# Optimization experiments

Hardware: AMD Instinct MI355X
Metric: run time of the kernel (lower is better)

## Reference

```python
import jax, jax.numpy as jnp
import numpy as np

H = 8   # n_heads
C = 2   # top-k scale factor: topk = int(C * log(L))


def setup_inputs() -> dict:
    key = jax.random.key(0)
    k1, k2, k3 = jax.random.split(key, 3)
    B, L, D = 16, 512, 4096  # L == D // H required by the original broadcasting
    Q = jax.random.normal(k1, (B, L, D), dtype=jnp.float32)
    K = jax.random.normal(k2, (B, L, D), dtype=jnp.float32)
    V = jax.random.normal(k3, (B, L, D), dtype=jnp.float32)
    return {"Q": Q, "K": K, "V": V}


def _autocorrelation(Q, K, V):
    B, L, D = Q.shape
    d = D // H
    # [B,L,D] -> [B,H,L,d]
    q = Q.reshape(B, L, H, d).transpose(0, 2, 1, 3)
    k = K.reshape(B, L, H, d).transpose(0, 2, 1, 3)
    v = V.reshape(B, L, H, d).transpose(0, 2, 1, 3)
    # FFT-based autocorrelation along the time axis (per head, per channel)
    qf = jnp.fft.fft(q, axis=2)
    kf = jnp.fft.fft(k, axis=2)
    corr = jnp.fft.ifft(qf * jnp.conj(kf), axis=2).real  # [B,H,L,d]
    topk = int(C * np.log(L))  # static: 12 for L=512
    # top-k delays per (batch, head, channel): move L to last axis
    w, idx = jax.lax.top_k(corr.transpose(0, 1, 3, 2), topk)  # [B,H,d,topk]
    w = jax.nn.softmax(w, axis=-1)
    pos = jnp.arange(L)[:, None]  # [L,1]
    out = jnp.zeros_like(v)       # [B,H,L,d]
    # small fixed loop over topk ~ O(log L) delays: gather + scale + accumulate
    for i in range(topk):
        g = jnp.minimum(idx[:, :, None, :, i] + pos, L - 1)        # [B,H,L,d]
        out = out + w[:, :, None, :, i] * jnp.take_along_axis(v, g, axis=2)
    return out.transpose(0, 2, 1, 3).reshape(B, L, D)


def reference(Q, K, V):
    return _autocorrelation(Q, K, V)
```

## Files before the change

### kernel.cpp

```cpp
#include <hip/hip_runtime.h>
#include <stdint.h>

#define L_LEN 512
#define D_DIM 4096
#define H_NUM 8
#define B_NUM 16
#define TOPK  12

typedef float f32x4 __attribute__((ext_vector_type(4)));


#define QA(G) (qbase + (((((uint32_t)(G)) & 127u) + ((((uint32_t)(G)) & 127u) >> 3)) << 4))

#define MAC4x16(QA_, QB_, QC_, QD_, QE_, KK_) do {                            \
    acc0  = fmaf(QA_.x, KK_.x, acc0);  acc0  = fmaf(QA_.y, KK_.y, acc0);      \
    acc0  = fmaf(QA_.z, KK_.z, acc0);  acc0  = fmaf(QA_.w, KK_.w, acc0);      \
    acc1  = fmaf(QA_.y, KK_.x, acc1);  acc1  = fmaf(QA_.z, KK_.y, acc1);      \
    acc1  = fmaf(QA_.w, KK_.z, acc1);  acc1  = fmaf(QB_.x, KK_.w, acc1);      \
    acc2  = fmaf(QA_.z, KK_.x, acc2);  acc2  = fmaf(QA_.w, KK_.y, acc2);      \
    acc2  = fmaf(QB_.x, KK_.z, acc2);  acc2  = fmaf(QB_.y, KK_.w, acc2);      \
    acc3  = fmaf(QA_.w, KK_.x, acc3);  acc3  = fmaf(QB_.x, KK_.y, acc3);      \
    acc3  = fmaf(QB_.y, KK_.z, acc3);  acc3  = fmaf(QB_.z, KK_.w, acc3);      \
    acc4  = fmaf(QB_.x, KK_.x, acc4);  acc4  = fmaf(QB_.y, KK_.y, acc4);      \
    acc4  = fmaf(QB_.z, KK_.z, acc4);  acc4  = fmaf(QB_.w, KK_.w, acc4);      \
    acc5  = fmaf(QB_.y, KK_.x, acc5);  acc5  = fmaf(QB_.z, KK_.y, acc5);      \
    acc5  = fmaf(QB_.w, KK_.z, acc5);  acc5  = fmaf(QC_.x, KK_.w, acc5);      \
    acc6  = fmaf(QB_.z, KK_.x, acc6);  acc6  = fmaf(QB_.w, KK_.y, acc6);      \
    acc6  = fmaf(QC_.x, KK_.z, acc6);  acc6  = fmaf(QC_.y, KK_.w, acc6);      \
    acc7  = fmaf(QB_.w, KK_.x, acc7);  acc7  = fmaf(QC_.x, KK_.y, acc7);      \
    acc7  = fmaf(QC_.y, KK_.z, acc7);  acc7  = fmaf(QC_.z, KK_.w, acc7);      \
    acc8  = fmaf(QC_.x, KK_.x, acc8);  acc8  = fmaf(QC_.y, KK_.y, acc8);      \
    acc8  = fmaf(QC_.z, KK_.z, acc8);  acc8  = fmaf(QC_.w, KK_.w, acc8);      \
    acc9  = fmaf(QC_.y, KK_.x, acc9);  acc9  = fmaf(QC_.z, KK_.y, acc9);      \
    acc9  = fmaf(QC_.w, KK_.z, acc9);  acc9  = fmaf(QD_.x, KK_.w, acc9);      \
    acc10 = fmaf(QC_.z, KK_.x, acc10); acc10 = fmaf(QC_.w, KK_.y, acc10);     \
    acc10 = fmaf(QD_.x, KK_.z, acc10); acc10 = fmaf(QD_.y, KK_.w, acc10);     \
    acc11 = fmaf(QC_.w, KK_.x, acc11); acc11 = fmaf(QD_.x, KK_.y, acc11);     \
    acc11 = fmaf(QD_.y, KK_.z, acc11); acc11 = fmaf(QD_.z, KK_.w, acc11);     \
    acc12 = fmaf(QD_.x, KK_.x, acc12); acc12 = fmaf(QD_.y, KK_.y, acc12);     \
    acc12 = fmaf(QD_.z, KK_.z, acc12); acc12 = fmaf(QD_.w, KK_.w, acc12);     \
    acc13 = fmaf(QD_.y, KK_.x, acc13); acc13 = fmaf(QD_.z, KK_.y, acc13);     \
    acc13 = fmaf(QD_.w, KK_.z, acc13); acc13 = fmaf(QE_.x, KK_.w, acc13);     \
    acc14 = fmaf(QD_.z, KK_.x, acc14); acc14 = fmaf(QD_.w, KK_.y, acc14);     \
    acc14 = fmaf(QE_.x, KK_.z, acc14); acc14 = fmaf(QE_.y, KK_.w, acc14);     \
    acc15 = fmaf(QD_.w, KK_.x, acc15); acc15 = fmaf(QE_.x, KK_.y, acc15);     \
    acc15 = fmaf(QE_.y, KK_.z, acc15); acc15 = fmaf(QE_.z, KK_.w, acc15);     \
  } while (0)

#define ITERX(A0,A1,A2,A3, B0,B1,B2,B3, C0,C1,C2,C3) do {                    \
    const uint32_t a0_ = QA(gnext);                                          \
    const uint32_t a1_ = QA(gnext + 1);                                      \
    const uint32_t a2_ = QA(gnext + 2);                                      \
    const uint32_t a3_ = QA(gnext + 3);                                      \
    asm volatile(                                                            \
      "ds_read_b128 %0, %8\n\t"                                              \
      "ds_read_b128 %1, %9\n\t"                                              \
      "ds_read_b128 %2, %10\n\t"                                             \
      "ds_read_b128 %3, %11\n\t"                                             \
      "ds_read_b128 %4, %12\n\t"                                             \
      "ds_read_b128 %5, %12 offset:16\n\t"                                   \
      "ds_read_b128 %6, %12 offset:32\n\t"                                   \
      "ds_read_b128 %7, %12 offset:48\n\t"                                   \
      "s_waitcnt lgkmcnt(0)"                                                 \
      : "=&v"(C0), "=&v"(C1), "=&v"(C2), "=&v"(C3),                          \
        "=&v"(k0), "=&v"(k1), "=&v"(k2), "=&v"(k3)                           \
      : "v"(a0_), "v"(a1_), "v"(a2_), "v"(a3_), "v"(kptr)                    \
      : "memory");                                                           \
    MAC4x16(A0, A1, A2, A3, B0, k0);                                         \
    MAC4x16(A1, A2, A3, B0, B1, k1);                                         \
    MAC4x16(A2, A3, B0, B1, B2, k2);                                         \
    MAC4x16(A3, B0, B1, B2, B3, k3);                                         \
    gnext += 4; kptr += 64;                                                  \
  } while (0)

__global__ __launch_bounds__(256, 4) void corr_topk_kernel(
    const float* __restrict__ Q, const float* __restrict__ K,
    float* __restrict__ ws_w, int* __restrict__ ws_i)
{
  __shared__ __align__(16) float qs[8][576];
  __shared__ __align__(16) float ks[8][512];

  const int tid = threadIdx.x;
  const int bid = blockIdx.x;
  const int work = (bid & 7) * 1024 + (bid >> 3);
  const int bh   = work >> 6;
  const int c0   = (work & 63) * 8;

  const size_t base = (size_t)(bh >> 3) * (size_t)(L_LEN * D_DIM)
                    + (size_t)(bh & 7) * 512 + c0;

  #pragma unroll
  for (int rep = 0; rep < 4; ++rep) {
    const int idx  = rep * 256 + tid;
    const int t    = idx >> 1;
    const int half = idx & 1;
    const float4 qv = *(const float4*)(Q + base + (size_t)t * D_DIM + half * 4);
    const float4 kv = *(const float4*)(K + base + (size_t)t * D_DIM + half * 4);
    const int g  = t >> 2;
    const int pw = ((g + (g >> 3)) << 2) | (t & 3);
    const int cb = half * 4;
    const float qa[4] = {qv.x, qv.y, qv.z, qv.w};
    const float ka[4] = {kv.x, kv.y, kv.z, kv.w};
    #pragma unroll
    for (int j = 0; j < 4; ++j) {
      qs[cb + j][pw] = qa[j];
      ks[cb + j][t]  = ka[j];
    }
  }
  __syncthreads();

  const int wv   = tid >> 6;
  const int lane = tid & 63;
  const int m    = lane & 31;
  const int ch   = wv * 2 + (lane >> 5);
  const int tau0 = m * 16;
  const int gq   = m * 4;

  const uint32_t qbase = (uint32_t)(uintptr_t)(&qs[ch][0]);
  uint32_t       kptr  = (uint32_t)(uintptr_t)(&ks[ch][0]);

  float acc0  = 0.f, acc1  = 0.f, acc2  = 0.f, acc3  = 0.f;
  float acc4  = 0.f, acc5  = 0.f, acc6  = 0.f, acc7  = 0.f;
  float acc8  = 0.f, acc9  = 0.f, acc10 = 0.f, acc11 = 0.f;
  float acc12 = 0.f, acc13 = 0.f, acc14 = 0.f, acc15 = 0.f;
  f32x4 wA0, wA1, wA2, wA3, wB0, wB1, wB2, wB3, wC0, wC1, wC2, wC3;
  f32x4 k0, k1, k2, k3;

  {
    const uint32_t p0 = QA(gq),     p1 = QA(gq + 1);
    const uint32_t p2 = QA(gq + 2), p3 = QA(gq + 3);
    const uint32_t p4 = QA(gq + 4), p5 = QA(gq + 5);
    const uint32_t p6 = QA(gq + 6), p7 = QA(gq + 7);
    asm volatile(
      "ds_read_b128 %0, %8\n\t"
      "ds_read_b128 %1, %9\n\t"
      "ds_read_b128 %2, %10\n\t"
      "ds_read_b128 %3, %11\n\t"
      "ds_read_b128 %4, %12\n\t"
      "ds_read_b128 %5, %13\n\t"
      "ds_read_b128 %6, %14\n\t"
      "ds_read_b128 %7, %15\n\t"
      "s_waitcnt lgkmcnt(0)"
      : "=&v"(wA0), "=&v"(wA1), "=&v"(wA2), "=&v"(wA3),
        "=&v"(wB0), "=&v"(wB1), "=&v"(wB2), "=&v"(wB3)
      : "v"(p0), "v"(p1), "v"(p2), "v"(p3), "v"(p4), "v"(p5), "v"(p6), "v"(p7)
      : "memory");
  }

  uint32_t gnext = (uint32_t)(gq + 8);

  #pragma unroll 1
  for (int i = 0; i < 30; i += 3) {
    ITERX(wA0,wA1,wA2,wA3, wB0,wB1,wB2,wB3, wC0,wC1,wC2,wC3);
    ITERX(wB0,wB1,wB2,wB3, wC0,wC1,wC2,wC3, wA0,wA1,wA2,wA3);
    ITERX(wC0,wC1,wC2,wC3, wA0,wA1,wA2,wA3, wB0,wB1,wB2,wB3);
  }
  ITERX(wA0,wA1,wA2,wA3, wB0,wB1,wB2,wB3, wC0,wC1,wC2,wC3);
  ITERX(wB0,wB1,wB2,wB3, wC0,wC1,wC2,wC3, wA0,wA1,wA2,wA3);

  float acc[16] = {acc0, acc1, acc2,  acc3,  acc4,  acc5,  acc6,  acc7,
                   acc8, acc9, acc10, acc11, acc12, acc13, acc14, acc15};

  float bv[TOPK]; int bi[TOPK];
  #pragma unroll
  for (int s = 0; s < TOPK; ++s) {
    float lv = acc[0]; int li = 0;
    #pragma unroll
    for (int i = 1; i < 16; ++i) if (acc[i] > lv) { lv = acc[i]; li = i; }
    int gi = tau0 + li;
    #pragma unroll
    for (int off = 16; off >= 1; off >>= 1) {
      const float ov = __shfl_xor(lv, off, 32);
      const int   oi = __shfl_xor(gi, off, 32);
      if (ov > lv || (ov == lv && oi < gi)) { lv = ov; gi = oi; }
    }
    bv[s] = lv; bi[s] = gi;
    const int slot = gi - tau0;
    #pragma unroll
    for (int i = 0; i < 16; ++i) acc[i] = (slot == i) ? -3.4e38f : acc[i];
  }

  float e[TOPK]; float sum = 0.f;
  #pragma unroll
  for (int s = 0; s < TOPK; ++s) { e[s] = expf(bv[s] - bv[0]); sum += e[s]; }
  const float inv = 1.f / sum;

  if (m == 0) {
    const int g = (bh * 512 + c0 + ch) * TOPK;
    #pragma unroll
    for (int s = 0; s < TOPK; ++s) { ws_w[g + s] = e[s] * inv; ws_i[g + s] = bi[s]; }
  }
}

__global__ __launch_bounds__(512, 4) void gather_kernel(
    const float* __restrict__ V, const float* __restrict__ ws_w,
    const int* __restrict__ ws_i, float* __restrict__ out)
{
  __shared__ __align__(16) float vs[512][32];

  const int tid = threadIdx.x;
  const int bid = blockIdx.x;
  const int work = (bid & 7) * 256 + (bid >> 3);
  const int b  = work >> 7;
  const int dg = work & 127;
  const int d0 = dg * 32;
  const int h  = d0 >> 9;
  const int c0 = d0 & 511;

  const size_t vcol = (size_t)b * (size_t)(L_LEN * D_DIM) + d0;

  const int cl   = tid & 31;
  const int tsub = tid >> 5;

  float4 stga, stgb;
  const int e0 = tid, e1 = 512 + tid;
  const int ra0 = e0 >> 3, qa0 = (e0 & 7) * 4;
  const int rb0 = e1 >> 3, qb0 = (e1 & 7) * 4;

  stga = *(const float4*)(V + vcol + (size_t)(384 + ra0) * D_DIM + qa0);
  stgb = *(const float4*)(V + vcol + (size_t)(384 + rb0) * D_DIM + qb0);

  const int g = ((b * 8 + h) * 512 + c0 + cl) * TOPK;
  float w[TOPK]; int r0[TOPK];
  #pragma unroll
  for (int s = 0; s < TOPK; ++s) { w[s] = ws_w[g + s]; r0[s] = ws_i[g + s]; }

  const size_t ob = vcol + cl;

  #pragma unroll 1
  for (int ph = 3; ph >= 0; --ph) {
    *(float4*)(&vs[ph * 128 + ra0][qa0]) = stga;
    *(float4*)(&vs[ph * 128 + rb0][qb0]) = stgb;
    if (ph > 0) {
      stga = *(const float4*)(V + vcol + (size_t)((ph - 1) * 128 + ra0) * D_DIM + qa0);
      stgb = *(const float4*)(V + vcol + (size_t)((ph - 1) * 128 + rb0) * D_DIM + qb0);
    }
    asm volatile("s_waitcnt lgkmcnt(0)" ::: "memory");
    __builtin_amdgcn_s_barrier();
    asm volatile("" ::: "memory");

    #pragma unroll
    for (int k8 = 0; k8 < 8; ++k8) {
      const int t = ph * 128 + (k8 << 4) + tsub;
      float a = 0.f;
      #pragma unroll
      for (int s = 0; s < TOPK; ++s) {
        int r = r0[s] + t;
        r = r > (L_LEN - 1) ? (L_LEN - 1) : r;
        a = fmaf(w[s], vs[r][cl], a);
      }
      out[ob + (size_t)t * D_DIM] = a;
    }
  }
}

extern "C" void kernel_launch(void* const* d_in, const int* in_sizes, int n_in,
                              void* d_out, int out_size, void* d_ws, size_t ws_size,
                              hipStream_t stream)
{
  const float* Q = (const float*)d_in[0];
  const float* K = (const float*)d_in[1];
  const float* V = (const float*)d_in[2];
  float* out = (float*)d_out;

  float* ws_w = (float*)d_ws;
  int*   ws_i = (int*)((char*)d_ws + (size_t)B_NUM * H_NUM * 512 * TOPK * sizeof(float));

  corr_topk_kernel<<<dim3(B_NUM * H_NUM * 64), dim3(256), 0, stream>>>(Q, K, ws_w, ws_i);
  gather_kernel<<<dim3(B_NUM * H_NUM * 16), dim3(512), 0, stream>>>(V, ws_w, ws_i, out);
}
```

Before: 765.3 us.

## Software-pipeline LDS reads in correlation loop with partial lgkmcnt waits

Replaces the block-load-then-wait-all inner loop with a rolling pipeline. Each MAC step waits only for its own operands via lgkmcnt(6), then issues the Q and K reads for a later step, so LDS latency overlaps with FMAs. The 12-register triple rotation becomes an 8-register ring plus four K registers. The shared arrays also get extra padding, which changes the LDS bank mapping. This relies on the order of the inline-asm ds_reads and on sched_barrier to keep the waitcnt counts correct, and the changed padding could alter bank conflicts.

```diff
diff --git a/kernel.cpp b/kernel.cpp
--- a/kernel.cpp
+++ b/kernel.cpp
@@ -47,38 +47,51 @@
     acc15 = fmaf(QE_.y, KK_.z, acc15); acc15 = fmaf(QE_.z, KK_.w, acc15);     \
   } while (0)
 
-#define ITERX(A0,A1,A2,A3, B0,B1,B2,B3, C0,C1,C2,C3) do {                    \
-    const uint32_t a0_ = QA(gnext);                                          \
-    const uint32_t a1_ = QA(gnext + 1);                                      \
-    const uint32_t a2_ = QA(gnext + 2);                                      \
-    const uint32_t a3_ = QA(gnext + 3);                                      \
-    asm volatile(                                                            \
-      "ds_read_b128 %0, %8\n\t"                                              \
-      "ds_read_b128 %1, %9\n\t"                                              \
-      "ds_read_b128 %2, %10\n\t"                                             \
-      "ds_read_b128 %3, %11\n\t"                                             \
-      "ds_read_b128 %4, %12\n\t"                                             \
-      "ds_read_b128 %5, %12 offset:16\n\t"                                   \
-      "ds_read_b128 %6, %12 offset:32\n\t"                                   \
-      "ds_read_b128 %7, %12 offset:48\n\t"                                   \
-      "s_waitcnt lgkmcnt(0)"                                                 \
-      : "=&v"(C0), "=&v"(C1), "=&v"(C2), "=&v"(C3),                          \
-        "=&v"(k0), "=&v"(k1), "=&v"(k2), "=&v"(k3)                           \
-      : "v"(a0_), "v"(a1_), "v"(a2_), "v"(a3_), "v"(kptr)                    \
-      : "memory");                                                           \
-    MAC4x16(A0, A1, A2, A3, B0, k0);                                         \
-    MAC4x16(A1, A2, A3, B0, B1, k1);                                         \
-    MAC4x16(A2, A3, B0, B1, B2, k2);                                         \
-    MAC4x16(A3, B0, B1, B2, B3, k3);                                         \
-    gnext += 4; kptr += 64;                                                  \
+#define WAITL(N) do {                                                         \
+    asm volatile("s_waitcnt lgkmcnt(" #N ")" ::: "memory");                   \
+    __builtin_amdgcn_sched_barrier(0);                                        \
+  } while (0)
+
+#define ISS2(QR, KR, KOFF) do {                                               \
+    const uint32_t qa_ = QA(gnext);                                           \
+    asm volatile(                                                             \
+      "ds_read_b128 %0, %2\n\t"                                               \
+      "ds_read_b128 %1, %3 offset:" #KOFF                                     \
+      : "=&v"(QR), "=&v"(KR)                                                  \
+      : "v"(qa_), "v"(kcur)                                                   \
+      : "memory");                                                            \
+    ++gnext;                                                                  \
+  } while (0)
+
+#define ESTEP do {                                                            \
+    WAITL(6); MAC4x16(R0,R1,R2,R3,R4, K0); ISS2(R0, K0, 64);                  \
+    WAITL(6); MAC4x16(R1,R2,R3,R4,R5, K1); ISS2(R1, K1, 80);                  \
+    WAITL(6); MAC4x16(R2,R3,R4,R5,R6, K2); ISS2(R2, K2, 96);                  \
+    WAITL(6); MAC4x16(R3,R4,R5,R6,R7, K3); ISS2(R3, K3, 112);                 \
+    kcur += 64;                                                               \
+  } while (0)
+
+#define OSTEP do {                                                            \
+    WAITL(6); MAC4x16(R4,R5,R6,R7,R0, K0); ISS2(R4, K0, 64);                  \
+    WAITL(6); MAC4x16(R5,R6,R7,R0,R1, K1); ISS2(R5, K1, 80);                  \
+    WAITL(6); MAC4x16(R6,R7,R0,R1,R2, K2); ISS2(R6, K2, 96);                  \
+    WAITL(6); MAC4x16(R7,R0,R1,R2,R3, K3); ISS2(R7, K3, 112);                 \
+    kcur += 64;                                                               \
+  } while (0)
+
+#define TSTEP do {                                                            \
+    WAITL(6); MAC4x16(R4,R5,R6,R7,R0, K0);                                    \
+    WAITL(4); MAC4x16(R5,R6,R7,R0,R1, K1);                                    \
+    WAITL(2); MAC4x16(R6,R7,R0,R1,R2, K2);                                    \
+    WAITL(0); MAC4x16(R7,R0,R1,R2,R3, K3);                                    \
   } while (0)
 
 __global__ __launch_bounds__(256, 4) void corr_topk_kernel(
     const float* __restrict__ Q, const float* __restrict__ K,
     float* __restrict__ ws_w, int* __restrict__ ws_i)
 {
-  __shared__ __align__(16) float qs[8][576];
-  __shared__ __align__(16) float ks[8][512];
+  __shared__ __align__(16) float qs[8][580];
+  __shared__ __align__(16) float ks[8][516];
 
   const int tid = threadIdx.x;
   const int bid = blockIdx.x;
@@ -117,14 +130,14 @@
   const int gq   = m * 4;
 
   const uint32_t qbase = (uint32_t)(uintptr_t)(&qs[ch][0]);
-  uint32_t       kptr  = (uint32_t)(uintptr_t)(&ks[ch][0]);
+  uint32_t       kcur  = (uint32_t)(uintptr_t)(&ks[ch][0]);
 
   float acc0  = 0.f, acc1  = 0.f, acc2  = 0.f, acc3  = 0.f;
   float acc4  = 0.f, acc5  = 0.f, acc6  = 0.f, acc7  = 0.f;
   float acc8  = 0.f, acc9  = 0.f, acc10 = 0.f, acc11 = 0.f;
   float acc12 = 0.f, acc13 = 0.f, acc14 = 0.f, acc15 = 0.f;
-  f32x4 wA0, wA1, wA2, wA3, wB0, wB1, wB2, wB3, wC0, wC1, wC2, wC3;
-  f32x4 k0, k1, k2, k3;
+  f32x4 R0, R1, R2, R3, R4, R5, R6, R7;
+  f32x4 K0, K1, K2, K3;
 
   {
     const uint32_t p0 = QA(gq),     p1 = QA(gq + 1);
@@ -132,31 +145,34 @@
     const uint32_t p4 = QA(gq + 4), p5 = QA(gq + 5);
     const uint32_t p6 = QA(gq + 6), p7 = QA(gq + 7);
     asm volatile(
-      "ds_read_b128 %0, %8\n\t"
-      "ds_read_b128 %1, %9\n\t"
-      "ds_read_b128 %2, %10\n\t"
-      "ds_read_b128 %3, %11\n\t"
-      "ds_read_b128 %4, %12\n\t"
-      "ds_read_b128 %5, %13\n\t"
-      "ds_read_b128 %6, %14\n\t"
-      "ds_read_b128 %7, %15\n\t"
-      "s_waitcnt lgkmcnt(0)"
-      : "=&v"(wA0), "=&v"(wA1), "=&v"(wA2), "=&v"(wA3),
-        "=&v"(wB0), "=&v"(wB1), "=&v"(wB2), "=&v"(wB3)
-      : "v"(p0), "v"(p1), "v"(p2), "v"(p3), "v"(p4), "v"(p5), "v"(p6), "v"(p7)
+      "ds_read_b128 %0, %12\n\t"
+      "ds_read_b128 %1, %13\n\t"
+      "ds_read_b128 %2, %14\n\t"
+      "ds_read_b128 %3, %15\n\t"
+      "ds_read_b128 %4, %16\n\t"
+      "ds_read_b128 %8, %20\n\t"
+      "ds_read_b128 %5, %17\n\t"
+      "ds_read_b128 %9, %20 offset:16\n\t"
+      "ds_read_b128 %6, %18\n\t"
+      "ds_read_b128 %10, %20 offset:32\n\t"
+      "ds_read_b128 %7, %19\n\t"
+      "ds_read_b128 %11, %20 offset:48"
+      : "=&v"(R0), "=&v"(R1), "=&v"(R2), "=&v"(R3),
+        "=&v"(R4), "=&v"(R5), "=&v"(R6), "=&v"(R7),
+        "=&v"(K0), "=&v"(K1), "=&v"(K2), "=&v"(K3)
+      : "v"(p0), "v"(p1), "v"(p2), "v"(p3), "v"(p4), "v"(p5), "v"(p6), "v"(p7),
+        "v"(kcur)
       : "memory");
   }
-
   uint32_t gnext = (uint32_t)(gq + 8);
 
   #pragma unroll 1
-  for (int i = 0; i < 30; i += 3) {
-    ITERX(wA0,wA1,wA2,wA3, wB0,wB1,wB2,wB3, wC0,wC1,wC2,wC3);
-    ITERX(wB0,wB1,wB2,wB3, wC0,wC1,wC2,wC3, wA0,wA1,wA2,wA3);
-    ITERX(wC0,wC1,wC2,wC3, wA0,wA1,wA2,wA3, wB0,wB1,wB2,wB3);
-  }
-  ITERX(wA0,wA1,wA2,wA3, wB0,wB1,wB2,wB3, wC0,wC1,wC2,wC3);
-  ITERX(wB0,wB1,wB2,wB3, wC0,wC1,wC2,wC3, wA0,wA1,wA2,wA3);
+  for (int it = 0; it < 15; ++it) {
+    ESTEP;
+    OSTEP;
+  }
+  ESTEP;
+  TSTEP;
 
   float acc[16] = {acc0, acc1, acc2,  acc3,  acc4,  acc5,  acc6,  acc7,
                    acc8, acc9, acc10, acc11, acc12, acc13, acc14, acc15};
```

Measured after the change: 785.4 us. 2.6% more time.
